# Kernel tuning notes

Measured on AMD Instinct MI355X. Metric: run time of the kernel, lower is better.

The kernel has to match this reference:

```python
import jax, jax.numpy as jnp
import numpy as np

DIM = 512
HEADS = 8
DIM_HEAD = 64  # scale constant from __init__; also dim // heads here
SCALE = DIM_HEAD ** -0.5


def setup_inputs() -> dict:
    key = jax.random.key(0)
    k1, k2, k3, k4 = jax.random.split(key, 4)
    x = jax.random.normal(k1, (2, 4096, DIM), dtype=jnp.float32)
    # nn.Linear weights: stored as [out, in]; we keep [in, out] for x @ W
    w_qkv = jax.random.normal(k2, (DIM, 3 * DIM), dtype=jnp.float32) * (DIM ** -0.5)
    w_out = jax.random.normal(k3, (DIM, DIM), dtype=jnp.float32) * (DIM ** -0.5)
    b_out = jax.random.normal(k4, (DIM,), dtype=jnp.float32) * 0.02
    return {"x": x, "w_qkv": w_qkv, "w_out": w_out, "b_out": b_out}


def reference(x, w_qkv, w_out, b_out):
    B, N, C = x.shape
    H = HEADS
    Dh = C // H
    qkv = x @ w_qkv                                   # [B, N, 3C]
    q, k, v = jnp.split(qkv, 3, axis=-1)
    # [B, N, C] -> [B, H, N, Dh]
    reshape = lambda t: t.reshape(B, N, H, Dh).transpose(0, 2, 1, 3)
    q, k, v = reshape(q), reshape(k), reshape(v)
    attn = jnp.einsum("bhnd,bhmd->bhnm", q, k) * SCALE  # [B, H, N, N]
    attn = jax.nn.softmax(attn, axis=-1)
    out = jnp.einsum("bhnm,bhmd->bhnd", attn, v)       # [B, H, N, Dh]
    out = out.transpose(0, 2, 1, 3).reshape(B, N, C)
    return out @ w_out + b_out
```

## Files before the change

### kernel.cpp

```cpp
#include <hip/hip_runtime.h>
#include <stdint.h>

typedef unsigned short u16;
typedef __bf16 bf16x8 __attribute__((ext_vector_type(8)));
typedef float fx4 __attribute__((ext_vector_type(4)));
typedef float fx16 __attribute__((ext_vector_type(16)));


__device__ __forceinline__ u16 f2bf(float f) {
    unsigned int u = __float_as_uint(f);
    u += 0x7fffu + ((u >> 16) & 1u);
    return (u16)(u >> 16);
}

__device__ __forceinline__ bf16x8 ld8(const u16* p) {
    return __builtin_bit_cast(bf16x8, *(const int4*)p);
}

__device__ __forceinline__ uint32_t pk2bf(float lo, float hi) {
    uint32_t a = __float_as_uint(lo) + 0x8000u;
    uint32_t b = __float_as_uint(hi) + 0x8000u;
    return __builtin_amdgcn_perm(b, a, 0x07060302u);
}

typedef __attribute__((address_space(3))) uint32_t lds_u32;
typedef __attribute__((address_space(1))) const uint32_t glb_u32;
__device__ __forceinline__ void glds16(const u16* g, u16* l) {
    __builtin_amdgcn_global_load_lds((glb_u32*)g, (lds_u32*)l, 16, 0, 0);
}


__global__ __launch_bounds__(256) void transpose_cast_kernel(const float* __restrict__ w_qkv,
                                                             u16* __restrict__ wqkv_t,
                                                             const float* __restrict__ w_out,
                                                             u16* __restrict__ wout_t) {
    __shared__ float T[64][65];
    int t = threadIdx.x;
    int bx = blockIdx.x;
    const float* in; u16* out; int NR = 512, NC;
    if (bx < 24) { in = w_qkv; out = wqkv_t; NC = 1536; }
    else         { in = w_out; out = wout_t; NC = 512; bx -= 24; }
    int i0 = blockIdx.y * 64, j0 = bx * 64;
    int r = t >> 4, cc = t & 15;
#pragma unroll
    for (int j = 0; j < 4; ++j) {
        int row = r + j * 16;
        float4 v = *(const float4*)(in + (size_t)(i0 + row) * NC + j0 + cc * 4);
        T[row][cc * 4 + 0] = v.x; T[row][cc * 4 + 1] = v.y;
        T[row][cc * 4 + 2] = v.z; T[row][cc * 4 + 3] = v.w;
    }
    __syncthreads();
#pragma unroll
    for (int j = 0; j < 4; ++j) {
        int jr = r + j * 16;
        unsigned int u0 = f2bf(T[cc * 4 + 0][jr]) | ((unsigned int)f2bf(T[cc * 4 + 1][jr]) << 16);
        unsigned int u1 = f2bf(T[cc * 4 + 2][jr]) | ((unsigned int)f2bf(T[cc * 4 + 3][jr]) << 16);
        uint2 u; u.x = u0; u.y = u1;
        *(uint2*)(out + (size_t)(j0 + jr) * NR + i0 + cc * 4) = u;
    }
}


#define QSCALE 0.180336880f

template<int MODE>
__global__ __launch_bounds__(256) void gemm_kernel(const void* __restrict__ Avoid,
                                                   const u16* __restrict__ Bt,
                                                   u16* __restrict__ Qf,
                                                   u16* __restrict__ Kf,
                                                   u16* __restrict__ Vf,
                                                   const float* __restrict__ bias,
                                                   float* __restrict__ Out,
                                                   int Ncols) {
    __shared__ __align__(16) u16 Sh[16384];
    int tid = threadIdx.x;
    int w = tid >> 6, lane = tid & 63;
    int m16 = lane & 15, quad = lane >> 4;
    int ntn = Ncols / 128;
    int bx = blockIdx.x % ntn, by = blockIdx.x / ntn;
    int r0 = by * 128, c0 = bx * 128;
    int wr = w >> 1, wc = w & 1;
    int lrow = lane >> 2, lchk = (lane & 3) * 8;

    fx4 acc[4][4] = {};

    for (int k0 = 0; k0 < 512; k0 += 32) {
        __syncthreads();
#pragma unroll
        for (int j = 0; j < 2; ++j) {
            int rw = j * 64 + w * 16;
            if (MODE == 0) {
                int L = tid + j * 256;
                int row = L >> 2, c = L & 3;
                const float* af = (const float*)Avoid + (size_t)(r0 + row) * 512 + k0 + c * 8;
                float4 a = *(const float4*)af, b = *(const float4*)(af + 4);
                int4 v;
                v.x = (int)pk2bf(a.x, a.y); v.y = (int)pk2bf(a.z, a.w);
                v.z = (int)pk2bf(b.x, b.y); v.w = (int)pk2bf(b.z, b.w);
                *(int4*)&Sh[row * 32 + c * 8] = v;
            } else {
                const u16* ab = (const u16*)Avoid;
                glds16(ab + (size_t)(r0 + rw + lrow) * 512 + k0 + lchk, &Sh[rw * 32]);
            }
            glds16(Bt + (size_t)(c0 + rw + lrow) * 512 + k0 + lchk, &Sh[4096 + rw * 32]);
        }
        __syncthreads();
        bf16x8 af[4], bfr[4];
#pragma unroll
        for (int t = 0; t < 4; ++t) {
            af[t]  = ld8(&Sh[(wr * 64 + t * 16 + m16) * 32 + quad * 8]);
            bfr[t] = ld8(&Sh[4096 + (wc * 64 + t * 16 + m16) * 32 + quad * 8]);
        }
#pragma unroll
        for (int mt = 0; mt < 4; ++mt)
#pragma unroll
            for (int nt = 0; nt < 4; ++nt)
                acc[mt][nt] = __builtin_amdgcn_mfma_f32_16x16x32_bf16(af[mt], bfr[nt], acc[mt][nt], 0, 0, 0);
    }

    if (MODE == 0) {
        int sec = c0 >> 9;
        __syncthreads();
        if (sec <= 1) {
            float sc = (sec == 0) ? QSCALE : 1.0f;
#pragma unroll
            for (int mt = 0; mt < 4; ++mt)
#pragma unroll
                for (int nt = 0; nt < 4; ++nt) {
                    int lb = wc * 16 + (wr * 2 + (mt >> 1)) * 4 + nt;
                    int eb = lb * 512 + (m16 >> 3) * 256 + ((mt & 1) * 16 + quad * 4) * 8 + (m16 & 7);
#pragma unroll
                    for (int r = 0; r < 4; ++r)
                        Sh[eb + r * 8] = f2bf(acc[mt][nt][r] * sc);
                }
        } else {
#pragma unroll
            for (int mt = 0; mt < 4; ++mt)
#pragma unroll
                for (int nt = 0; nt < 4; ++nt) {
                    int lb = wc * 16 + wr * 8 + (nt >> 1) * 4 + mt;
                    int eb = lb * 512 + (quad & 1) * 256 + ((nt & 1) * 16 + m16) * 8 + (quad >> 1) * 4;
                    unsigned int u0 = f2bf(acc[mt][nt][0]) | ((unsigned int)f2bf(acc[mt][nt][1]) << 16);
                    unsigned int u1 = f2bf(acc[mt][nt][2]) | ((unsigned int)f2bf(acc[mt][nt][3]) << 16);
                    uint2 u; u.x = u0; u.y = u1;
                    *(uint2*)&Sh[eb] = u;
                }
        }
        __syncthreads();
        int b_ = r0 >> 12, n0 = r0 & 4095, hd0 = (c0 >> 6) & 7;
        u16* dst; size_t gb0;
        if (sec == 0)      { dst = Qf; gb0 = (size_t)(n0 >> 5) * 2048; }
        else if (sec == 1) { dst = Kf; gb0 = (size_t)(n0 >> 5) * 2048; }
        else               { dst = Vf; gb0 = (size_t)(n0 >> 6) * 4096; }
        int hl = tid >> 7;
        size_t gbase = (size_t)(b_ * 8 + hd0 + hl) * 262144 + gb0 + (size_t)(tid & 127) * 64;
#pragma unroll
        for (int s = 0; s < 8; ++s)
            *(int4*)(dst + gbase + s * 8) = *(const int4*)&Sh[tid * 64 + s * 8];
    } else {
#pragma unroll
        for (int mt = 0; mt < 4; ++mt) {
            int R0 = r0 + wr * 64 + mt * 16 + quad * 4;
#pragma unroll
            for (int nt = 0; nt < 4; ++nt) {
                int C = c0 + wc * 64 + nt * 16 + m16;
                float bv = bias[C];
#pragma unroll
                for (int r = 0; r < 4; ++r)
                    Out[(size_t)(R0 + r) * 512 + C] = acc[mt][nt][r] + bv;
            }
        }
    }
}


__device__ __forceinline__ void attn_iter(bf16x8 (&KC)[2][4], bf16x8 (&KN)[2][4],
                                          const bf16x8 (&qf)[4], const bf16x8& onesA,
                                          const fx16& Z,
                                          fx16& O0, fx16& O1, fx16& Lacc,
                                          const u16* __restrict__ Kh,
                                          const u16* __restrict__ Vh,
                                          int lane, int K0) {
    bf16x8 vf[2][4];
    {
        const u16* vb = Vh + (size_t)(K0 >> 6) * 4096 + lane * 8;
#pragma unroll
        for (int dt = 0; dt < 2; ++dt)
#pragma unroll
            for (int ch = 0; ch < 4; ++ch)
                vf[dt][ch] = ld8(vb + (dt * 4 + ch) * 512);
    }
    {
        int kn0 = (K0 + 64) & 4095;
        const u16* kb = Kh + (size_t)(kn0 >> 5) * 2048 + lane * 8;
#pragma unroll
        for (int dc = 0; dc < 4; ++dc) {
            KN[0][dc] = ld8(kb + dc * 512);
            KN[1][dc] = ld8(kb + 2048 + dc * 512);
        }
    }
    fx16 S0 = Z, S1 = Z;
#pragma unroll
    for (int dc = 0; dc < 4; ++dc) {
        S0 = __builtin_amdgcn_mfma_f32_32x32x16_bf16(KC[0][dc], qf[dc], S0, 0, 0, 0);
        S1 = __builtin_amdgcn_mfma_f32_32x32x16_bf16(KC[1][dc], qf[dc], S1, 0, 0, 0);
    }
    uint32_t pk0[8], pk1[8];
#pragma unroll
    for (int i = 0; i < 8; ++i) {
        pk0[i] = pk2bf(__builtin_amdgcn_exp2f(S0[2 * i]), __builtin_amdgcn_exp2f(S0[2 * i + 1]));
        pk1[i] = pk2bf(__builtin_amdgcn_exp2f(S1[2 * i]), __builtin_amdgcn_exp2f(S1[2 * i + 1]));
    }
#pragma unroll
    for (int c = 0; c < 4; ++c) {
        const uint32_t* pk = (c < 2) ? pk0 : pk1;
        int o = (c & 1) * 4;
        int4 bi; bi.x = (int)pk[o]; bi.y = (int)pk[o + 1]; bi.z = (int)pk[o + 2]; bi.w = (int)pk[o + 3];
        bf16x8 bfrag = __builtin_bit_cast(bf16x8, bi);
        O0 = __builtin_amdgcn_mfma_f32_32x32x16_bf16(vf[0][c], bfrag, O0, 0, 0, 0);
        O1 = __builtin_amdgcn_mfma_f32_32x32x16_bf16(vf[1][c], bfrag, O1, 0, 0, 0);
        Lacc = __builtin_amdgcn_mfma_f32_32x32x16_bf16(onesA, bfrag, Lacc, 0, 0, 0);
    }
}

__global__ __launch_bounds__(256, 2) void attn_kernel(const u16* __restrict__ Qf,
                                                      const u16* __restrict__ Kf,
                                                      const u16* __restrict__ Vf,
                                                      u16* __restrict__ Ob) {
    __shared__ __align__(16) u16 Eo[4 * 32 * 68];

    int tid = threadIdx.x;
    int w = tid >> 6, lane = tid & 63;
    int q32 = lane & 31, h = lane >> 5;
    int bh = ((blockIdx.x & 7) << 1) | ((blockIdx.x >> 3) & 1);
    int qt = blockIdx.x >> 4;
    int q0 = qt * 128;

    const u16* Qh = Qf + (size_t)bh * 262144;
    const u16* Kh = Kf + (size_t)bh * 262144;
    const u16* Vh = Vf + (size_t)bh * 262144;

    bf16x8 qf[4];
    {
        const u16* qb = Qh + (size_t)(qt * 4 + w) * 2048 + lane * 8;
#pragma unroll
        for (int dc = 0; dc < 4; ++dc)
            qf[dc] = ld8(qb + dc * 512);
    }

    int4 oi; oi.x = oi.y = oi.z = oi.w = 0x3F803F80;
    const bf16x8 onesA = __builtin_bit_cast(bf16x8, oi);
    const fx16 Z = {};
    fx16 O0 = {}, O1 = {}, Lacc = {};

    bf16x8 kA[2][4], kB[2][4];
    {
        const u16* kb = Kh + lane * 8;
#pragma unroll
        for (int dc = 0; dc < 4; ++dc) {
            kA[0][dc] = ld8(kb + dc * 512);
            kA[1][dc] = ld8(kb + 2048 + dc * 512);
        }
    }

    for (int k0 = 0; k0 < 4096; k0 += 128) {
        asm volatile("s_barrier" ::: "memory");
        attn_iter(kA, kB, qf, onesA, Z, O0, O1, Lacc, Kh, Vh, lane, k0);
        attn_iter(kB, kA, qf, onesA, Z, O0, O1, Lacc, Kh, Vh, lane, k0 + 64);
    }

    float inv = 1.0f / Lacc[0];
    int ebase = w * 2176 + q32 * 68;
#pragma unroll
    for (int i = 0; i < 8; ++i) {
        int dbase = 8 * (i >> 1) + (i & 1) * 2 + 4 * h;
        uint32_t p0 = pk2bf(O0[2 * i] * inv, O0[2 * i + 1] * inv);
        uint32_t p1 = pk2bf(O1[2 * i] * inv, O1[2 * i + 1] * inv);
        *(uint32_t*)&Eo[ebase + dbase]      = p0;
        *(uint32_t*)&Eo[ebase + dbase + 32] = p1;
    }
    __syncthreads();
    int row = lane >> 1, half = lane & 1;
    int rb = w * 2176 + row * 68 + half * 32;
    int b = bh >> 3, hh = bh & 7;
    size_t gb = ((size_t)(b * 4096 + q0 + w * 32 + row)) * 512 + hh * 64 + half * 32;
#pragma unroll
    for (int s = 0; s < 4; ++s) {
        uint2 a = *(const uint2*)&Eo[rb + s * 8];
        uint2 c = *(const uint2*)&Eo[rb + s * 8 + 4];
        int4 v; v.x = (int)a.x; v.y = (int)a.y; v.z = (int)c.x; v.w = (int)c.y;
        *(int4*)(Ob + gb + s * 8) = v;
    }
}


extern "C" void kernel_launch(void* const* d_in, const int* in_sizes, int n_in,
                              void* d_out, int out_size, void* d_ws, size_t ws_size,
                              hipStream_t stream) {
    const float* x     = (const float*)d_in[0];
    const float* w_qkv = (const float*)d_in[1];
    const float* w_out = (const float*)d_in[2];
    const float* b_out = (const float*)d_in[3];
    float* out = (float*)d_out;

    char* ws = (char*)d_ws;
    u16* wqkv_t = (u16*)(ws);
    u16* wout_t = (u16*)(ws + 1572864);
    u16* Qfb    = (u16*)(ws + 2097152);
    u16* Kfb    = (u16*)(ws + 10485760);
    u16* Vfb    = (u16*)(ws + 18874368);
    u16* Ob     = (u16*)(ws + 27262976);

    transpose_cast_kernel<<<dim3(32, 8), 256, 0, stream>>>(w_qkv, wqkv_t, w_out, wout_t);
    gemm_kernel<0><<<768, 256, 0, stream>>>(x, wqkv_t, Qfb, Kfb, Vfb, nullptr, nullptr, 1536);
    attn_kernel<<<512, 256, 0, stream>>>(Qfb, Kfb, Vfb, Ob);
    gemm_kernel<1><<<256, 256, 0, stream>>>(Ob, wout_t, nullptr, nullptr, nullptr, b_out, out, 512);
}
```

Measured before the change: 220.1 us.

## Pre-cast x to bf16, remap GEMM blocks per XCD, stage K tiles in LDS

Adds a separate kernel that casts x to bf16, so the QKV GEMM can load A through global_load_lds like the output GEMM instead of converting fp32 inside the K-loop. Both GEMMs now map block IDs so that consecutive blocks on the same XCD share row tiles, which should improve L2 reuse. The attention kernel stops holding K fragments double-buffered in registers and instead loads each K tile into a double-buffered LDS buffer shared by the four waves, with a block barrier per 64-key step. The trade-offs are an extra launch plus an 8 MB round trip for x, and more synchronisation in attention in exchange for fewer redundant K loads and lower register pressure.

Result: no change. 216.5 us (-1.7%).

```diff
diff --git a/kernel.cpp b/kernel.cpp
--- a/kernel.cpp
+++ b/kernel.cpp
@@ -27,6 +27,18 @@
 typedef __attribute__((address_space(1))) const uint32_t glb_u32;
 __device__ __forceinline__ void glds16(const u16* g, u16* l) {
     __builtin_amdgcn_global_load_lds((glb_u32*)g, (lds_u32*)l, 16, 0, 0);
+}
+
+
+__global__ __launch_bounds__(256) void cast_x_kernel(const float* __restrict__ x,
+                                                     u16* __restrict__ xb) {
+    int idx = blockIdx.x * 256 + threadIdx.x;
+    const float4* p = (const float4*)(x + (size_t)idx * 8);
+    float4 a = p[0], b = p[1];
+    int4 v;
+    v.x = (int)pk2bf(a.x, a.y); v.y = (int)pk2bf(a.z, a.w);
+    v.z = (int)pk2bf(b.x, b.y); v.w = (int)pk2bf(b.z, b.w);
+    *(int4*)(xb + (size_t)idx * 8) = v;
 }
 
 
@@ -64,7 +76,7 @@
 #define QSCALE 0.180336880f
 
 template<int MODE>
-__global__ __launch_bounds__(256) void gemm_kernel(const void* __restrict__ Avoid,
+__global__ __launch_bounds__(256) void gemm_kernel(const u16* __restrict__ A,
                                                    const u16* __restrict__ Bt,
                                                    u16* __restrict__ Qf,
                                                    u16* __restrict__ Kf,
@@ -77,7 +89,10 @@
     int w = tid >> 6, lane = tid & 63;
     int m16 = lane & 15, quad = lane >> 4;
     int ntn = Ncols / 128;
-    int bx = blockIdx.x % ntn, by = blockIdx.x / ntn;
+    int g = blockIdx.x;
+    int xcd = g & 7, j = g >> 3;
+    int by = xcd + 8 * (j / ntn);
+    int bx = j % ntn;
     int r0 = by * 128, c0 = bx * 128;
     int wr = w >> 1, wc = w & 1;
     int lrow = lane >> 2, lchk = (lane & 3) * 8;
@@ -87,21 +102,9 @@
     for (int k0 = 0; k0 < 512; k0 += 32) {
         __syncthreads();
 #pragma unroll
-        for (int j = 0; j < 2; ++j) {
-            int rw = j * 64 + w * 16;
-            if (MODE == 0) {
-                int L = tid + j * 256;
-                int row = L >> 2, c = L & 3;
-                const float* af = (const float*)Avoid + (size_t)(r0 + row) * 512 + k0 + c * 8;
-                float4 a = *(const float4*)af, b = *(const float4*)(af + 4);
-                int4 v;
-                v.x = (int)pk2bf(a.x, a.y); v.y = (int)pk2bf(a.z, a.w);
-                v.z = (int)pk2bf(b.x, b.y); v.w = (int)pk2bf(b.z, b.w);
-                *(int4*)&Sh[row * 32 + c * 8] = v;
-            } else {
-                const u16* ab = (const u16*)Avoid;
-                glds16(ab + (size_t)(r0 + rw + lrow) * 512 + k0 + lchk, &Sh[rw * 32]);
-            }
+        for (int jj = 0; jj < 2; ++jj) {
+            int rw = jj * 64 + w * 16;
+            glds16(A  + (size_t)(r0 + rw + lrow) * 512 + k0 + lchk, &Sh[rw * 32]);
             glds16(Bt + (size_t)(c0 + rw + lrow) * 512 + k0 + lchk, &Sh[4096 + rw * 32]);
         }
         __syncthreads();
@@ -174,59 +177,11 @@
 }
 
 
-__device__ __forceinline__ void attn_iter(bf16x8 (&KC)[2][4], bf16x8 (&KN)[2][4],
-                                          const bf16x8 (&qf)[4], const bf16x8& onesA,
-                                          const fx16& Z,
-                                          fx16& O0, fx16& O1, fx16& Lacc,
-                                          const u16* __restrict__ Kh,
-                                          const u16* __restrict__ Vh,
-                                          int lane, int K0) {
-    bf16x8 vf[2][4];
-    {
-        const u16* vb = Vh + (size_t)(K0 >> 6) * 4096 + lane * 8;
-#pragma unroll
-        for (int dt = 0; dt < 2; ++dt)
-#pragma unroll
-            for (int ch = 0; ch < 4; ++ch)
-                vf[dt][ch] = ld8(vb + (dt * 4 + ch) * 512);
-    }
-    {
-        int kn0 = (K0 + 64) & 4095;
-        const u16* kb = Kh + (size_t)(kn0 >> 5) * 2048 + lane * 8;
-#pragma unroll
-        for (int dc = 0; dc < 4; ++dc) {
-            KN[0][dc] = ld8(kb + dc * 512);
-            KN[1][dc] = ld8(kb + 2048 + dc * 512);
-        }
-    }
-    fx16 S0 = Z, S1 = Z;
-#pragma unroll
-    for (int dc = 0; dc < 4; ++dc) {
-        S0 = __builtin_amdgcn_mfma_f32_32x32x16_bf16(KC[0][dc], qf[dc], S0, 0, 0, 0);
-        S1 = __builtin_amdgcn_mfma_f32_32x32x16_bf16(KC[1][dc], qf[dc], S1, 0, 0, 0);
-    }
-    uint32_t pk0[8], pk1[8];
-#pragma unroll
-    for (int i = 0; i < 8; ++i) {
-        pk0[i] = pk2bf(__builtin_amdgcn_exp2f(S0[2 * i]), __builtin_amdgcn_exp2f(S0[2 * i + 1]));
-        pk1[i] = pk2bf(__builtin_amdgcn_exp2f(S1[2 * i]), __builtin_amdgcn_exp2f(S1[2 * i + 1]));
-    }
-#pragma unroll
-    for (int c = 0; c < 4; ++c) {
-        const uint32_t* pk = (c < 2) ? pk0 : pk1;
-        int o = (c & 1) * 4;
-        int4 bi; bi.x = (int)pk[o]; bi.y = (int)pk[o + 1]; bi.z = (int)pk[o + 2]; bi.w = (int)pk[o + 3];
-        bf16x8 bfrag = __builtin_bit_cast(bf16x8, bi);
-        O0 = __builtin_amdgcn_mfma_f32_32x32x16_bf16(vf[0][c], bfrag, O0, 0, 0, 0);
-        O1 = __builtin_amdgcn_mfma_f32_32x32x16_bf16(vf[1][c], bfrag, O1, 0, 0, 0);
-        Lacc = __builtin_amdgcn_mfma_f32_32x32x16_bf16(onesA, bfrag, Lacc, 0, 0, 0);
-    }
-}
-
 __global__ __launch_bounds__(256, 2) void attn_kernel(const u16* __restrict__ Qf,
                                                       const u16* __restrict__ Kf,
                                                       const u16* __restrict__ Vf,
                                                       u16* __restrict__ Ob) {
+    __shared__ __align__(16) u16 Ks[2][4096];
     __shared__ __align__(16) u16 Eo[4 * 32 * 68];
 
     int tid = threadIdx.x;
@@ -253,20 +208,57 @@
     const fx16 Z = {};
     fx16 O0 = {}, O1 = {}, Lacc = {};
 
-    bf16x8 kA[2][4], kB[2][4];
-    {
-        const u16* kb = Kh + lane * 8;
+    glds16(Kh + w * 1024 + lane * 8,       &Ks[0][w * 1024]);
+    glds16(Kh + w * 1024 + 512 + lane * 8, &Ks[0][w * 1024 + 512]);
+    __syncthreads();
+
+    for (int it = 0; it < 64; ++it) {
+        int K0 = it << 6;
+        int cur = it & 1, nxt = cur ^ 1;
+        {
+            int kn = (K0 + 64) & 4095;
+            const u16* ks = Kh + (size_t)kn * 64 + w * 1024 + lane * 8;
+            glds16(ks,       &Ks[nxt][w * 1024]);
+            glds16(ks + 512, &Ks[nxt][w * 1024 + 512]);
+        }
+        bf16x8 vf[2][4];
+        {
+            const u16* vb = Vh + (size_t)K0 * 64 + lane * 8;
+#pragma unroll
+            for (int dt = 0; dt < 2; ++dt)
+#pragma unroll
+                for (int ch = 0; ch < 4; ++ch)
+                    vf[dt][ch] = ld8(vb + (dt * 4 + ch) * 512);
+        }
+        bf16x8 kf[2][4];
 #pragma unroll
         for (int dc = 0; dc < 4; ++dc) {
-            kA[0][dc] = ld8(kb + dc * 512);
-            kA[1][dc] = ld8(kb + 2048 + dc * 512);
-        }
-    }
-
-    for (int k0 = 0; k0 < 4096; k0 += 128) {
-        asm volatile("s_barrier" ::: "memory");
-        attn_iter(kA, kB, qf, onesA, Z, O0, O1, Lacc, Kh, Vh, lane, k0);
-        attn_iter(kB, kA, qf, onesA, Z, O0, O1, Lacc, Kh, Vh, lane, k0 + 64);
+            kf[0][dc] = ld8(&Ks[cur][dc * 512 + lane * 8]);
+            kf[1][dc] = ld8(&Ks[cur][2048 + dc * 512 + lane * 8]);
+        }
+        fx16 S0 = Z, S1 = Z;
+#pragma unroll
+        for (int dc = 0; dc < 4; ++dc) {
+            S0 = __builtin_amdgcn_mfma_f32_32x32x16_bf16(kf[0][dc], qf[dc], S0, 0, 0, 0);
+            S1 = __builtin_amdgcn_mfma_f32_32x32x16_bf16(kf[1][dc], qf[dc], S1, 0, 0, 0);
+        }
+        uint32_t pk0[8], pk1[8];
+#pragma unroll
+        for (int i = 0; i < 8; ++i) {
+            pk0[i] = pk2bf(__builtin_amdgcn_exp2f(S0[2 * i]), __builtin_amdgcn_exp2f(S0[2 * i + 1]));
+            pk1[i] = pk2bf(__builtin_amdgcn_exp2f(S1[2 * i]), __builtin_amdgcn_exp2f(S1[2 * i + 1]));
+        }
+#pragma unroll
+        for (int c = 0; c < 4; ++c) {
+            const uint32_t* pk = (c < 2) ? pk0 : pk1;
+            int o = (c & 1) * 4;
+            int4 bi; bi.x = (int)pk[o]; bi.y = (int)pk[o + 1]; bi.z = (int)pk[o + 2]; bi.w = (int)pk[o + 3];
+            bf16x8 bfrag = __builtin_bit_cast(bf16x8, bi);
+            O0 = __builtin_amdgcn_mfma_f32_32x32x16_bf16(vf[0][c], bfrag, O0, 0, 0, 0);
+            O1 = __builtin_amdgcn_mfma_f32_32x32x16_bf16(vf[1][c], bfrag, O1, 0, 0, 0);
+            Lacc = __builtin_amdgcn_mfma_f32_32x32x16_bf16(onesA, bfrag, Lacc, 0, 0, 0);
+        }
+        __syncthreads();
     }
 
     float inv = 1.0f / Lacc[0];
@@ -304,15 +296,17 @@
     float* out = (float*)d_out;
 
     char* ws = (char*)d_ws;
-    u16* wqkv_t = (u16*)(ws);
-    u16* wout_t = (u16*)(ws + 1572864);
-    u16* Qfb    = (u16*)(ws + 2097152);
-    u16* Kfb    = (u16*)(ws + 10485760);
-    u16* Vfb    = (u16*)(ws + 18874368);
-    u16* Ob     = (u16*)(ws + 27262976);
-
+    u16* x_b    = (u16*)(ws);
+    u16* wqkv_t = (u16*)(ws + 8388608);
+    u16* wout_t = (u16*)(ws + 9961472);
+    u16* Qfb    = (u16*)(ws + 10485760);
+    u16* Kfb    = (u16*)(ws + 18874368);
+    u16* Vfb    = (u16*)(ws + 27262976);
+    u16* Ob     = (u16*)(ws + 35651584);
+
+    cast_x_kernel<<<2048, 256, 0, stream>>>(x, x_b);
     transpose_cast_kernel<<<dim3(32, 8), 256, 0, stream>>>(w_qkv, wqkv_t, w_out, wout_t);
-    gemm_kernel<0><<<768, 256, 0, stream>>>(x, wqkv_t, Qfb, Kfb, Vfb, nullptr, nullptr, 1536);
+    gemm_kernel<0><<<768, 256, 0, stream>>>(x_b, wqkv_t, Qfb, Kfb, Vfb, nullptr, nullptr, 1536);
     attn_kernel<<<512, 256, 0, stream>>>(Qfb, Kfb, Vfb, Ob);
     gemm_kernel<1><<<256, 256, 0, stream>>>(Ob, wout_t, nullptr, nullptr, nullptr, b_out, out, 512);
 }
```

## Split attention over two KV halves, precast x, and swizzle GEMM blocks

Applied to the files above, without the earlier changes.

Attention now runs 1024 blocks, each covering half of the keys. Each block writes unnormalized fp32 partial outputs and row sums to the workspace, and a new combine kernel adds the two halves, normalizes and writes bf16. The goal is more parallelism and better wave occupancy. Separately, x is cast to bf16 in its own kernel so the QKV GEMM can load A with global-to-LDS loads. GEMM block indices are also remapped so rows are grouped by XCD. This adds extra launches and partial-result traffic, and the Part buffer aliases x_b in the workspace.

After: 229.8 us. 1.04x slower.

```diff
diff --git a/kernel.cpp b/kernel.cpp
--- a/kernel.cpp
+++ b/kernel.cpp
@@ -27,6 +27,18 @@
 typedef __attribute__((address_space(1))) const uint32_t glb_u32;
 __device__ __forceinline__ void glds16(const u16* g, u16* l) {
     __builtin_amdgcn_global_load_lds((glb_u32*)g, (lds_u32*)l, 16, 0, 0);
+}
+
+
+__global__ __launch_bounds__(256) void cast_x_kernel(const float* __restrict__ x,
+                                                     u16* __restrict__ xb) {
+    int idx = blockIdx.x * 256 + threadIdx.x;
+    const float4* p = (const float4*)(x + (size_t)idx * 8);
+    float4 a = p[0], b = p[1];
+    int4 v;
+    v.x = (int)pk2bf(a.x, a.y); v.y = (int)pk2bf(a.z, a.w);
+    v.z = (int)pk2bf(b.x, b.y); v.w = (int)pk2bf(b.z, b.w);
+    *(int4*)(xb + (size_t)idx * 8) = v;
 }
 
 
@@ -64,7 +76,7 @@
 #define QSCALE 0.180336880f
 
 template<int MODE>
-__global__ __launch_bounds__(256) void gemm_kernel(const void* __restrict__ Avoid,
+__global__ __launch_bounds__(256) void gemm_kernel(const u16* __restrict__ A,
                                                    const u16* __restrict__ Bt,
                                                    u16* __restrict__ Qf,
                                                    u16* __restrict__ Kf,
@@ -77,7 +89,10 @@
     int w = tid >> 6, lane = tid & 63;
     int m16 = lane & 15, quad = lane >> 4;
     int ntn = Ncols / 128;
-    int bx = blockIdx.x % ntn, by = blockIdx.x / ntn;
+    int g = blockIdx.x;
+    int xcd = g & 7, j = g >> 3;
+    int by = xcd + 8 * (j / ntn);
+    int bx = j % ntn;
     int r0 = by * 128, c0 = bx * 128;
     int wr = w >> 1, wc = w & 1;
     int lrow = lane >> 2, lchk = (lane & 3) * 8;
@@ -87,21 +102,9 @@
     for (int k0 = 0; k0 < 512; k0 += 32) {
         __syncthreads();
 #pragma unroll
-        for (int j = 0; j < 2; ++j) {
-            int rw = j * 64 + w * 16;
-            if (MODE == 0) {
-                int L = tid + j * 256;
-                int row = L >> 2, c = L & 3;
-                const float* af = (const float*)Avoid + (size_t)(r0 + row) * 512 + k0 + c * 8;
-                float4 a = *(const float4*)af, b = *(const float4*)(af + 4);
-                int4 v;
-                v.x = (int)pk2bf(a.x, a.y); v.y = (int)pk2bf(a.z, a.w);
-                v.z = (int)pk2bf(b.x, b.y); v.w = (int)pk2bf(b.z, b.w);
-                *(int4*)&Sh[row * 32 + c * 8] = v;
-            } else {
-                const u16* ab = (const u16*)Avoid;
-                glds16(ab + (size_t)(r0 + rw + lrow) * 512 + k0 + lchk, &Sh[rw * 32]);
-            }
+        for (int jj = 0; jj < 2; ++jj) {
+            int rw = jj * 64 + w * 16;
+            glds16(A  + (size_t)(r0 + rw + lrow) * 512 + k0 + lchk, &Sh[rw * 32]);
             glds16(Bt + (size_t)(c0 + rw + lrow) * 512 + k0 + lchk, &Sh[4096 + rw * 32]);
         }
         __syncthreads();
@@ -191,7 +194,7 @@
                 vf[dt][ch] = ld8(vb + (dt * 4 + ch) * 512);
     }
     {
-        int kn0 = (K0 + 64) & 4095;
+        int kn0 = (K0 + 64) & 2047;
         const u16* kb = Kh + (size_t)(kn0 >> 5) * 2048 + lane * 8;
 #pragma unroll
         for (int dc = 0; dc < 4; ++dc) {
@@ -226,19 +229,16 @@
 __global__ __launch_bounds__(256, 2) void attn_kernel(const u16* __restrict__ Qf,
                                                       const u16* __restrict__ Kf,
                                                       const u16* __restrict__ Vf,
-                                                      u16* __restrict__ Ob) {
-    __shared__ __align__(16) u16 Eo[4 * 32 * 68];
-
+                                                      float* __restrict__ Part) {
     int tid = threadIdx.x;
     int w = tid >> 6, lane = tid & 63;
-    int q32 = lane & 31, h = lane >> 5;
     int bh = ((blockIdx.x & 7) << 1) | ((blockIdx.x >> 3) & 1);
-    int qt = blockIdx.x >> 4;
-    int q0 = qt * 128;
+    int half = (blockIdx.x >> 4) & 1;
+    int qt = blockIdx.x >> 5;
 
     const u16* Qh = Qf + (size_t)bh * 262144;
-    const u16* Kh = Kf + (size_t)bh * 262144;
-    const u16* Vh = Vf + (size_t)bh * 262144;
+    const u16* Kh = Kf + (size_t)bh * 262144 + (size_t)half * 131072;
+    const u16* Vh = Vf + (size_t)bh * 262144 + (size_t)half * 131072;
 
     bf16x8 qf[4];
     {
@@ -263,27 +263,56 @@
         }
     }
 
-    for (int k0 = 0; k0 < 4096; k0 += 128) {
-        asm volatile("s_barrier" ::: "memory");
+    for (int k0 = 0; k0 < 2048; k0 += 128) {
         attn_iter(kA, kB, qf, onesA, Z, O0, O1, Lacc, Kh, Vh, lane, k0);
         attn_iter(kB, kA, qf, onesA, Z, O0, O1, Lacc, Kh, Vh, lane, k0 + 64);
     }
 
-    float inv = 1.0f / Lacc[0];
+    float* dst = Part + (size_t)(blockIdx.x * 4 + w) * 33 * 64 + lane;
+#pragma unroll
+    for (int r = 0; r < 16; ++r) {
+        dst[r * 64]        = O0[r];
+        dst[(16 + r) * 64] = O1[r];
+    }
+    dst[32 * 64] = Lacc[0];
+}
+
+
+__global__ __launch_bounds__(256) void combine_kernel(const float* __restrict__ Part,
+                                                      u16* __restrict__ Ob) {
+    __shared__ __align__(16) u16 Eo[4 * 32 * 68];
+    int tid = threadIdx.x;
+    int w = tid >> 6, lane = tid & 63;
+    int q32 = lane & 31, h = lane >> 5;
+    int bhcode = blockIdx.x & 15, qt = blockIdx.x >> 4;
+    int bh = ((bhcode & 7) << 1) | (bhcode >> 3);
+    int q0 = qt * 128;
+    int p0 = (qt << 5) | bhcode, p1 = p0 | 16;
+
+    const float* s0 = Part + (size_t)(p0 * 4 + w) * 33 * 64 + lane;
+    const float* s1 = Part + (size_t)(p1 * 4 + w) * 33 * 64 + lane;
+    float O0[16], O1[16];
+#pragma unroll
+    for (int r = 0; r < 16; ++r) {
+        O0[r] = s0[r * 64] + s1[r * 64];
+        O1[r] = s0[(16 + r) * 64] + s1[(16 + r) * 64];
+    }
+    float inv = 1.0f / (s0[32 * 64] + s1[32 * 64]);
+
     int ebase = w * 2176 + q32 * 68;
 #pragma unroll
     for (int i = 0; i < 8; ++i) {
         int dbase = 8 * (i >> 1) + (i & 1) * 2 + 4 * h;
-        uint32_t p0 = pk2bf(O0[2 * i] * inv, O0[2 * i + 1] * inv);
-        uint32_t p1 = pk2bf(O1[2 * i] * inv, O1[2 * i + 1] * inv);
-        *(uint32_t*)&Eo[ebase + dbase]      = p0;
-        *(uint32_t*)&Eo[ebase + dbase + 32] = p1;
+        uint32_t v0 = pk2bf(O0[2 * i] * inv, O0[2 * i + 1] * inv);
+        uint32_t v1 = pk2bf(O1[2 * i] * inv, O1[2 * i + 1] * inv);
+        *(uint32_t*)&Eo[ebase + dbase]      = v0;
+        *(uint32_t*)&Eo[ebase + dbase + 32] = v1;
     }
     __syncthreads();
-    int row = lane >> 1, half = lane & 1;
-    int rb = w * 2176 + row * 68 + half * 32;
+    int row = lane >> 1, halfc = lane & 1;
+    int rb = w * 2176 + row * 68 + halfc * 32;
     int b = bh >> 3, hh = bh & 7;
-    size_t gb = ((size_t)(b * 4096 + q0 + w * 32 + row)) * 512 + hh * 64 + half * 32;
+    size_t gb = ((size_t)(b * 4096 + q0 + w * 32 + row)) * 512 + hh * 64 + halfc * 32;
 #pragma unroll
     for (int s = 0; s < 4; ++s) {
         uint2 a = *(const uint2*)&Eo[rb + s * 8];
@@ -304,15 +333,19 @@
     float* out = (float*)d_out;
 
     char* ws = (char*)d_ws;
-    u16* wqkv_t = (u16*)(ws);
-    u16* wout_t = (u16*)(ws + 1572864);
-    u16* Qfb    = (u16*)(ws + 2097152);
-    u16* Kfb    = (u16*)(ws + 10485760);
-    u16* Vfb    = (u16*)(ws + 18874368);
-    u16* Ob     = (u16*)(ws + 27262976);
-
+    float* Part  = (float*)(ws);
+    u16* x_b     = (u16*)(ws);
+    u16* wqkv_t  = (u16*)(ws + 8388608);
+    u16* Qfb     = (u16*)(ws + 34603008);
+    u16* Kfb     = (u16*)(ws + 42991616);
+    u16* Vfb     = (u16*)(ws + 51380224);
+    u16* Ob      = (u16*)(ws + 59768832);
+    u16* wout_t  = (u16*)(ws + 68157440);
+
+    cast_x_kernel<<<2048, 256, 0, stream>>>(x, x_b);
     transpose_cast_kernel<<<dim3(32, 8), 256, 0, stream>>>(w_qkv, wqkv_t, w_out, wout_t);
-    gemm_kernel<0><<<768, 256, 0, stream>>>(x, wqkv_t, Qfb, Kfb, Vfb, nullptr, nullptr, 1536);
-    attn_kernel<<<512, 256, 0, stream>>>(Qfb, Kfb, Vfb, Ob);
+    gemm_kernel<0><<<768, 256, 0, stream>>>(x_b, wqkv_t, Qfb, Kfb, Vfb, nullptr, nullptr, 1536);
+    attn_kernel<<<1024, 256, 0, stream>>>(Qfb, Kfb, Vfb, Part);
+    combine_kernel<<<512, 256, 0, stream>>>(Part, Ob);
     gemm_kernel<1><<<256, 256, 0, stream>>>(Ob, wout_t, nullptr, nullptr, nullptr, b_out, out, 512);
 }
```
